# Performance work log

Measured on AMD Instinct MI355X. Metric: run time of the kernel, lower is better.

The kernel has to match this reference:

```python
import jax, jax.numpy as jnp
import numpy as np

B, T, H, L = 8, 256, 64, 3
NB, NF, HP = 17, 68, 6
K = 9  # temporal kernel
PAD = (K - 1) // 2
EPS = 1e-5


def _normalize(adj):
    adj = adj + np.eye(adj.shape[0], dtype=np.float32)
    d = adj.sum(1)
    dinv = np.power(d, -0.5)
    dinv[np.isinf(dinv)] = 0.0
    return (dinv[:, None] * adj * dinv[None, :]).astype(np.float32)


def _body_adj():
    a = np.zeros((NB, NB), np.float32)
    conns = [(0, 1), (0, 2), (1, 3), (2, 4), (0, 5), (0, 6), (5, 6), (5, 7), (7, 9), (6, 8), (8, 10), (5, 11), (6, 12), (11, 12), (11, 13), (13, 15), (12, 14), (14, 16)]
    for i, j in conns:
        a[i, j] = 1.0
        a[j, i] = 1.0
    return _normalize(a)


def _face_adj():
    a = np.zeros((NF, NF), np.float32)
    for i in range(16): a[i, i + 1] = 1.0
    for i in range(17, 21): a[i, i + 1] = 1.0
    for i in range(22, 26): a[i, i + 1] = 1.0
    for i in range(27, 30): a[i, i + 1] = 1.0
    for i in range(31, 35): a[i, i + 1] = 1.0
    for i in range(36, 41): a[i, i + 1] = 1.0
    a[41, 36] = 1.0
    for i in range(42, 47): a[i, i + 1] = 1.0
    a[47, 42] = 1.0
    for i in range(48, 59): a[i, i + 1] = 1.0
    a[59, 48] = 1.0
    for i in range(60, 67): a[i, i + 1] = 1.0
    a[67, 60] = 1.0
    a = a + a.T
    return _normalize(a)


def setup_inputs() -> dict:
    keys = iter(jax.random.split(jax.random.key(0), 80))

    def rn(shape, s):
        return jax.random.normal(next(keys), shape, jnp.float32) * s

    inp = {}
    inp['body_kps'] = jax.random.normal(next(keys), (B, T, NB * 2), jnp.float32)
    inp['face_kps_2d'] = jax.random.normal(next(keys), (B, T, NF * 2), jnp.float32)
    inp['head_pose'] = jax.random.normal(next(keys), (B, T, HP), jnp.float32)
    inp['body_adj'] = jnp.asarray(_body_adj())
    inp['face_adj'] = jnp.asarray(_face_adj())
    inp['body_proj_w'] = rn((2, H), 0.5)
    inp['body_proj_b'] = jnp.zeros((H,), jnp.float32)
    inp['face_proj_w'] = rn((2, H), 0.5)
    inp['face_proj_b'] = jnp.zeros((H,), jnp.float32)
    inp['head_w'] = rn((HP, H), 0.3)
    inp['head_b'] = jnp.zeros((H,), jnp.float32)
    for p in ('b', 'f'):
        inp[p + '_t1w'] = rn((L, H, H, K), 0.04)
        inp[p + '_t1b'] = jnp.zeros((L, H), jnp.float32)
        inp[p + '_bn1g'] = jnp.ones((L, H), jnp.float32)
        inp[p + '_bn1b'] = jnp.zeros((L, H), jnp.float32)
        inp[p + '_bn1m'] = rn((L, H), 0.1)
        inp[p + '_bn1v'] = jax.random.uniform(next(keys), (L, H), jnp.float32, 0.5, 1.5)
        inp[p + '_gcw'] = rn((L, H, H), 0.1)
        inp[p + '_gcb'] = jnp.zeros((L, H), jnp.float32)
        inp[p + '_t2w'] = rn((L, H, H, K), 0.04)
        inp[p + '_t2b'] = jnp.zeros((L, H), jnp.float32)
        inp[p + '_bn2g'] = jnp.ones((L, H), jnp.float32)
        inp[p + '_bn2b'] = jnp.zeros((L, H), jnp.float32)
        inp[p + '_bn2m'] = rn((L, H), 0.1)
        inp[p + '_bn2v'] = jax.random.uniform(next(keys), (L, H), jnp.float32, 0.5, 1.5)
    total = NB * H + NF * H + H  # 5504
    inp['fus1_w'] = rn((total, 4 * H), 0.02)
    inp['fus1_b'] = jnp.zeros((4 * H,), jnp.float32)
    inp['fus2_w'] = rn((4 * H, 2 * H), 0.06)
    inp['fus2_b'] = jnp.zeros((2 * H,), jnp.float32)
    inp['fus3_w'] = rn((2 * H, H), 0.09)
    inp['fus3_b'] = jnp.zeros((H,), jnp.float32)
    inp['fus4_w'] = rn((H, 5), 0.12)
    inp['fus4_b'] = jnp.zeros((5,), jnp.float32)
    return inp


def _conv_bn(x, w, b, g, be, m, v):
    # x: (BN, C, T); w: (O, I, K). Conv1d (pad=4) + eval-mode BatchNorm1d.
    y = jax.lax.conv_general_dilated(x, w, (1,), [(PAD, PAD)], dimension_numbers=('NCH', 'OIH', 'NCH'))
    y = y + b[None, :, None]
    inv = g * jax.lax.rsqrt(v + EPS)
    return y * inv[None, :, None] + (be - m * inv)[None, :, None]


def _block(x, adj, t1w, t1b, g1, b1, m1, v1, gw, gb, t2w, t2b, g2, b2, m2, v2):
    # x: (B, N, C, T); residual is identity (in_channels == out_channels)
    Bn, N, C, Tn = x.shape
    res = x
    h = jax.nn.relu(_conv_bn(x.reshape(Bn * N, C, Tn), t1w, t1b, g1, b1, m1, v1)).reshape(Bn, N, C, Tn)
    # spatial graph conv, batched over all timesteps at once (adj @ (x W) + b)
    support = jnp.einsum('bnct,co->bnot', h, gw)
    h = jax.nn.relu(jnp.einsum('mn,bnot->bmot', adj, support) + gb[None, None, :, None])
    h = _conv_bn(h.reshape(Bn * N, C, Tn), t2w, t2b, g2, b2, m2, v2).reshape(Bn, N, C, Tn)
    return h + res  # dropout = identity in eval


def _stream(x, n_nodes, pw, pb, adj, ps):
    Bn, Tn, _ = x.shape
    h = x.reshape(Bn, Tn, n_nodes, 2) @ pw + pb          # (B, T, N, H)
    h = jnp.transpose(h, (0, 2, 3, 1))                   # (B, N, H, T)
    for l in range(ps[0].shape[0]):
        h = _block(h, adj, *(p[l] for p in ps))
    return h.mean(axis=3).reshape(Bn, -1)                # temporal mean-pool, flatten nodes


def reference(body_kps, face_kps_2d, head_pose, body_adj, face_adj, body_proj_w, body_proj_b, face_proj_w, face_proj_b, head_w, head_b, b_t1w, b_t1b, b_bn1g, b_bn1b, b_bn1m, b_bn1v, b_gcw, b_gcb, b_t2w, b_t2b, b_bn2g, b_bn2b, b_bn2m, b_bn2v, f_t1w, f_t1b, f_bn1g, f_bn1b, f_bn1m, f_bn1v, f_gcw, f_gcb, f_t2w, f_t2b, f_bn2g, f_bn2b, f_bn2m, f_bn2v, fus1_w, fus1_b, fus2_w, fus2_b, fus3_w, fus3_b, fus4_w, fus4_b):
    bps = (b_t1w, b_t1b, b_bn1g, b_bn1b, b_bn1m, b_bn1v, b_gcw, b_gcb, b_t2w, b_t2b, b_bn2g, b_bn2b, b_bn2m, b_bn2v)
    fps = (f_t1w, f_t1b, f_bn1g, f_bn1b, f_bn1m, f_bn1v, f_gcw, f_gcb, f_t2w, f_t2b, f_bn2g, f_bn2b, f_bn2m, f_bn2v)
    bf = _stream(body_kps, NB, body_proj_w, body_proj_b, body_adj, bps)
    ff = _stream(face_kps_2d, NF, face_proj_w, face_proj_b, face_adj, fps)
    hp = jax.nn.relu(head_pose @ head_w + head_b).mean(axis=1)
    feat = jnp.concatenate([bf, ff, hp], axis=-1)
    h = jax.nn.relu(feat @ fus1_w + fus1_b)
    h = jax.nn.relu(h @ fus2_w + fus2_b)
    h = jax.nn.relu(h @ fus3_w + fus3_b)
    return h @ fus4_w + fus4_b
```

## Files before the change

kernel.cpp:

```cpp
#include <hip/hip_runtime.h>

constexpr int B_ = 8, T_ = 256, H_ = 64, L_ = 3, NB_ = 17, NF_ = 68, HP_ = 6, K_ = 9;
constexpr int FEAT_DIM = NB_ * H_ + NF_ * H_ + H_;
constexpr int HT = H_ * T_;

typedef _Float16 half4_t __attribute__((ext_vector_type(4)));
typedef _Float16 half8_t __attribute__((ext_vector_type(8)));
typedef float f32x16 __attribute__((ext_vector_type(16)));
typedef float f32x4 __attribute__((ext_vector_type(4)));

constexpr size_t SZ_AB = (size_t)B_ * NB_ * HT;
constexpr size_t SZ_AF = (size_t)B_ * NF_ * HT;
constexpr size_t OFF_TB   = 0;
constexpr size_t OFF_TF   = OFF_TB + SZ_AB / 2;
constexpr size_t OFF_SUPB = OFF_TF + SZ_AF / 2;
constexpr size_t OFF_SUPF = OFF_SUPB + SZ_AB / 2;
constexpr size_t OFF_GB   = OFF_SUPF + SZ_AF / 2;
constexpr size_t OFF_GF   = OFF_GB + SZ_AB / 2;
constexpr size_t OFF_W3   = OFF_GF + SZ_AF / 2;
constexpr size_t OFF_GW3  = OFF_W3 + 4 * 55296;
constexpr size_t OFF_B2   = OFF_GW3 + 2 * 6144;
constexpr size_t OFF_ADJPB= OFF_B2 + 768;
constexpr size_t OFF_ADJPF= OFF_ADJPB + 512;
constexpr size_t OFF_FEAT = OFF_ADJPF + 3840;
constexpr size_t OFF_P1   = OFF_FEAT + (size_t)B_ * FEAT_DIM;

struct ConvPrepSet { const float *w, *tb, *g, *bb, *m, *v; };

struct Args {
    const float *body_kps, *face_kps, *head_pose, *body_adj, *face_adj;
    const float *body_pw, *body_pb, *face_pw, *face_pb, *head_w, *head_b;
    ConvPrepSet sb1, sb2, sf1, sf2;
    const float *b_gcw, *f_gcw, *b_gcb, *f_gcb;
    const float *fus1_w, *fus1_b, *fus2_w, *fus2_b, *fus3_w, *fus3_b, *fus4_w, *fus4_b;
    _Float16 *TrB, *TrF, *SupB, *SupF, *Gb, *Gf;
    _Float16 *W3, *GW3, *adjPB, *adjPF;
    float *B2, *p1, *feat;
    float *out;
};

__device__ __forceinline__ half8_t ld_b8(const _Float16* p) {
    half4_t lo = *(const half4_t*)p;
    half4_t hi = *(const half4_t*)(p + 4);
    return __builtin_shufflevector(lo, hi, 0, 1, 2, 3, 4, 5, 6, 7);
}

__device__ __forceinline__ void st_b8(_Float16* p, half8_t v) {
    half4_t lo, hi;
#pragma unroll
    for (int j = 0; j < 4; ++j) { lo[j] = v[j]; hi[j] = v[4 + j]; }
    *(half4_t*)p = lo;
    *(half4_t*)(p + 4) = hi;
}

__device__ __forceinline__ void stage_chunk64(const _Float16* __restrict__ xb,
                                              _Float16* __restrict__ Xs, int tc, int tid) {
    for (int u = tid; u < 72 * 8; u += 256) {
        int row = u >> 3, c = u & 7;
        int t = tc * 64 + row - 4;
        half8_t v;
        if (t >= 0 && t < T_) {
            v = *(const half8_t*)(xb + (size_t)t * H_ + c * 8);
        } else {
#pragma unroll
            for (int j = 0; j < 8; ++j) v[j] = (_Float16)0.f;
        }
        st_b8(&Xs[row * 68 + c * 8], v);
    }
}

__device__ __forceinline__ void stage_res64(const _Float16* __restrict__ xb,
                                            _Float16* __restrict__ Rs, int tc, int tid) {
    for (int u = tid; u < 64 * 8; u += 256) {
        int row = u >> 3, c = u & 7;
        half8_t v = *(const half8_t*)(xb + (size_t)(tc * 64 + row) * H_ + c * 8);
        st_b8(&Rs[row * 68 + c * 8], v);
    }
}

__device__ __forceinline__ void conv_kloop(const half8_t* __restrict__ wl,
                                           const _Float16* __restrict__ Xs,
                                           int trow, int ln31, int kg, int ot,
                                           f32x16& acc) {
    const _Float16* xr0 = Xs + (size_t)(trow + ln31) * 68;
#pragma unroll
    for (int tap = 0; tap < K_; ++tap) {
#pragma unroll
        for (int ks = 0; ks < 4; ++ks) {
            int i8 = ks * 2 + kg;
            half8_t a = wl[(tap * 8 + i8) * H_ + ot * 32 + ln31];
            half8_t bf = ld_b8(xr0 + tap * 68 + i8 * 8);
            acc = __builtin_amdgcn_mfma_f32_32x32x16_f16(a, bf, acc, 0, 0, 0);
        }
    }
}

__device__ void convmix_core(const half8_t* __restrict__ wl,
                             const float* __restrict__ b1l,
                             const half8_t* __restrict__ gl,
                             _Float16* __restrict__ supb,
                             int tc, _Float16* __restrict__ Xs, int tid) {
    int ln = tid & 63;
    int w = __builtin_amdgcn_readfirstlane(tid >> 6);
    int ln31 = ln & 31, kg = ln >> 5;
    int ts = w & 1, ot = w >> 1;
    int trow = ts * 32;

    f32x16 acc;
#pragma unroll
    for (int r = 0; r < 16; ++r) acc[r] = 0.f;

    conv_kloop(wl, Xs, trow, ln31, kg, ot, acc);
    __syncthreads();

    _Float16* mrow = Xs + (size_t)(4 + trow + ln31) * 68;
#pragma unroll
    for (int rg = 0; rg < 4; ++rg) {
        int o0 = ot * 32 + rg * 8 + kg * 4;
        f32x4 bv = *(const f32x4*)(b1l + o0);
        half4_t hv;
#pragma unroll
        for (int j = 0; j < 4; ++j)
            hv[j] = (_Float16)fmaxf(acc[rg * 4 + j] + bv[j], 0.f);
        *(half4_t*)(mrow + o0) = hv;
    }
    __syncthreads();

    f32x16 acc2;
#pragma unroll
    for (int r = 0; r < 16; ++r) acc2[r] = 0.f;
#pragma unroll
    for (int ks = 0; ks < 4; ++ks) {
        int i8 = ks * 2 + kg;
        half8_t a = gl[i8 * H_ + ot * 32 + ln31];
        half8_t bf = ld_b8(mrow + i8 * 8);
        acc2 = __builtin_amdgcn_mfma_f32_32x32x16_f16(a, bf, acc2, 0, 0, 0);
    }
    __syncthreads();

#pragma unroll
    for (int rg = 0; rg < 4; ++rg) {
        int o0 = ot * 32 + rg * 8 + kg * 4;
        half4_t hv;
#pragma unroll
        for (int j = 0; j < 4; ++j)
            hv[j] = (_Float16)acc2[rg * 4 + j];
        *(half4_t*)(mrow + o0) = hv;
    }
    __syncthreads();
    _Float16* gout = supb + (size_t)(tc * 64) * H_;
    const _Float16* srow = Xs + 4 * 68;
#pragma unroll
    for (int k2 = 0; k2 < 2; ++k2) {
        int u = k2 * 256 + tid;
        int r = u >> 3, c = u & 7;
        half8_t v = ld_b8(srow + r * 68 + c * 8);
        *(half8_t*)(gout + (size_t)r * H_ + c * 8) = v;
    }
}

__global__ __launch_bounds__(256) void prep_k(Args A) {
    int blk = blockIdx.x;
    int tid = threadIdx.x;
    if (blk < 1728) {
        int set = blk / 432;
        int bx = blk % 432;
        ConvPrepSet s = (set == 0) ? A.sb1 : (set == 1) ? A.sb2 : (set == 2) ? A.sf1 : A.sf2;
        int idx = bx * 256 + tid;
        int k = idx % K_; int r = idx / K_;
        int i = r % H_; r /= H_;
        int o = r % H_; int l = r / H_;
        float sc = s.g[l * H_ + o] * rsqrtf(s.v[l * H_ + o] + 1e-5f);
        A.W3[(size_t)set * 110592 + ((((l * K_ + k) * 8 + (i >> 3)) * H_ + o) * 8) + (i & 7)]
            = (_Float16)(s.w[idx] * sc);
        if (i == 0 && k == 0)
            A.B2[set * 192 + l * H_ + o] =
                s.tb[l * H_ + o] * sc + s.bb[l * H_ + o] - s.m[l * H_ + o] * sc;
    } else if (blk < 1824) {
        int set = (blk - 1728) / 48;
        int bx = (blk - 1728) % 48;
        const float* gw = set ? A.f_gcw : A.b_gcw;
        int idx = bx * 256 + tid;
        int o = idx % H_; int r = idx / H_;
        int c = r % H_; int l = r / H_;
        A.GW3[(size_t)set * 12288 + (((l * 8 + (c >> 3)) * H_ + o) * 8) + (c & 7)]
            = (_Float16)gw[idx];
    } else {
        int idx = (blk - 1824) * 256 + tid;
        if (idx < 1024) {
            int m = idx >> 5, k = idx & 31;
            A.adjPB[idx] = (m < NB_ && k < NB_) ? (_Float16)A.body_adj[m * NB_ + k] : (_Float16)0.f;
        } else if (idx < 8704) {
            int j = idx - 1024;
            int m = j / 80, k = j % 80;
            A.adjPF[j] = (m < NF_ && k < NF_) ? (_Float16)A.face_adj[m * NF_ + k] : (_Float16)0.f;
        } else if (idx < 10752) {
            A.p1[idx - 8704] = 0.f;
        } else if (idx < 10752 + B_ * FEAT_DIM) {
            A.feat[idx - 10752] = 0.f;
        }
    }
}

__global__ __launch_bounds__(256, 8) void projcm_k(Args A) {
    __shared__ __align__(16) _Float16 Xs[72 * 68];
    int blk = blockIdx.x, tid = threadIdx.x;
    bool isB = blk < 4 * B_ * NB_;
    int j = isB ? blk : blk - 4 * B_ * NB_;
    int bn = j >> 2, tc = j & 3;
    const float* kps = isB ? A.body_kps : A.face_kps;
    const float* pw  = isB ? A.body_pw  : A.face_pw;
    const float* pb  = isB ? A.body_pb  : A.face_pb;
    _Float16* trunk  = isB ? A.TrB : A.TrF;
    int N = isB ? NB_ : NF_;
    int b = bn / N, n = bn % N;

    if (tid < 144) {
        int row = tid >> 1, hf = tid & 1;
        int t = tc * 64 + row - 4;
        _Float16* xr = Xs + row * 68 + hf * 32;
        if (t >= 0 && t < T_) {
            float x0 = kps[((size_t)b * T_ + t) * (N * 2) + n * 2 + 0];
            float x1 = kps[((size_t)b * T_ + t) * (N * 2) + n * 2 + 1];
            bool own = (row >= 4 && row < 68);
            _Float16* ob = trunk + (size_t)bn * HT + (size_t)t * H_ + hf * 32;
#pragma unroll
            for (int cg2 = 0; cg2 < 4; ++cg2) {
                half8_t v;
#pragma unroll
                for (int jj = 0; jj < 8; ++jj) {
                    int c = hf * 32 + cg2 * 8 + jj;
                    v[jj] = (_Float16)fmaf(x0, pw[c], fmaf(x1, pw[H_ + c], pb[c]));
                }
                st_b8(xr + cg2 * 8, v);
                if (own) *(half8_t*)(ob + cg2 * 8) = v;
            }
        } else {
            half8_t z;
#pragma unroll
            for (int jj = 0; jj < 8; ++jj) z[jj] = (_Float16)0.f;
            st_b8(xr, z);
            st_b8(xr + 8, z);
            st_b8(xr + 16, z);
            st_b8(xr + 24, z);
        }
    }
    __syncthreads();

    const half8_t* w1 = (const half8_t*)(A.W3 + (isB ? 0 : 221184));
    const float* b1l  = isB ? A.B2 : A.B2 + 384;
    const half8_t* gl = (const half8_t*)(A.GW3 + (isB ? 0 : 12288));
    _Float16* supb = (isB ? A.SupB : A.SupF) + (size_t)bn * HT;
    convmix_core(w1, b1l, gl, supb, tc, Xs, tid);
}

__global__ __launch_bounds__(256, 8) void cm_k(Args A, int l) {
    __shared__ __align__(16) _Float16 Xs[72 * 68];
    int blk = blockIdx.x, tid = threadIdx.x;
    bool isB = blk < 4 * B_ * NB_;
    int j = isB ? blk : blk - 4 * B_ * NB_;
    int bn = j >> 2, tc = j & 3;
    const _Float16* trunk = isB ? A.TrB : A.TrF;

    stage_chunk64(trunk + (size_t)bn * HT, Xs, tc, tid);
    __syncthreads();

    const half8_t* w1 = (const half8_t*)(A.W3 + (isB ? 0 : 221184)) + (size_t)l * (K_ * 8 * H_);
    const float* b1l  = (isB ? A.B2 : A.B2 + 384) + l * H_;
    const half8_t* gl = (const half8_t*)(A.GW3 + (isB ? 0 : 12288)) + (size_t)l * (8 * H_);
    _Float16* supb = (isB ? A.SupB : A.SupF) + (size_t)bn * HT;
    convmix_core(w1, b1l, gl, supb, tc, Xs, tid);
}

template <int N, int MT, int KS>
__device__ void adjmix_impl(const _Float16* __restrict__ sup,
                            const half8_t* __restrict__ adjP,
                            const float* __restrict__ gb,
                            _Float16* __restrict__ out,
                            int blk, int l, _Float16* Ls, int tid) {
    constexpr int KP = KS * 16;
    constexpr int PITCH = KP + 4;
    int b = blk >> 7, cb = blk & 127;
    int colbase = cb * 128;

    for (int u = tid; u < KP * 16; u += 256) {
        int n = u >> 4, cs = u & 15;
        half8_t v;
        if (n < N) v = *(const half8_t*)(sup + (size_t)(b * N + n) * HT + colbase + cs * 8);
        else {
#pragma unroll
            for (int j = 0; j < 8; ++j) v[j] = (_Float16)0.f;
        }
#pragma unroll
        for (int j = 0; j < 8; ++j) Ls[(cs * 8 + j) * PITCH + n] = v[j];
    }
    __syncthreads();

    int ln = tid & 63;
    int w = __builtin_amdgcn_readfirstlane(tid >> 6);
    int ln31 = ln & 31, kg = ln >> 5;
    int colL = w * 32 + ln31;

    f32x16 acc[MT];
#pragma unroll
    for (int mt = 0; mt < MT; ++mt)
#pragma unroll
        for (int r = 0; r < 16; ++r) acc[mt][r] = 0.f;

#pragma unroll
    for (int ks = 0; ks < KS; ++ks) {
        half8_t bf = ld_b8(&Ls[colL * PITCH + ks * 16 + kg * 8]);
#pragma unroll
        for (int mt = 0; mt < MT; ++mt) {
            half8_t af = adjP[(size_t)(mt * 32 + ln31) * (KP / 8) + ks * 2 + kg];
            acc[mt] = __builtin_amdgcn_mfma_f32_32x32x16_f16(af, bf, acc[mt], 0, 0, 0);
        }
    }
    __syncthreads();

    float gbv = gb[l * H_ + (colL & 63)];
#pragma unroll
    for (int mt = 0; mt < MT; ++mt) {
#pragma unroll
        for (int r = 0; r < 16; ++r) {
            int m = mt * 32 + (r & 3) + 8 * (r >> 2) + 4 * kg;
            Ls[m * 132 + colL] = (_Float16)fmaxf(acc[mt][r] + gbv, 0.f);
        }
    }
    __syncthreads();

    for (int u = tid; u < N * 16; u += 256) {
        int m = u >> 4, c = u & 15;
        half8_t v = ld_b8(&Ls[m * 132 + c * 8]);
        *(half8_t*)(out + (size_t)(b * N + m) * HT + colbase + c * 8) = v;
    }
}

__global__ __launch_bounds__(256) void adjmix_k(Args A, int l) {
    __shared__ __align__(16) _Float16 Ls[12800];
    int blk = blockIdx.x, tid = threadIdx.x;
    if (blk < 1024)
        adjmix_impl<NB_, 1, 2>(A.SupB, (const half8_t*)A.adjPB, A.b_gcb, A.Gb, blk, l, Ls, tid);
    else
        adjmix_impl<NF_, 3, 5>(A.SupF, (const half8_t*)A.adjPF, A.f_gcb, A.Gf, blk - 1024, l, Ls, tid);
}

__global__ __launch_bounds__(256, 8) void c2_k(Args A, int l) {
    __shared__ __align__(16) _Float16 Xs[72 * 68];
    __shared__ __align__(16) _Float16 Rs[64 * 68];
    int blk = blockIdx.x, tid = threadIdx.x;
    bool isB = blk < 4 * B_ * NB_;
    int j = isB ? blk : blk - 4 * B_ * NB_;
    int bn = j >> 2, tc = j & 3;
    const _Float16* G = isB ? A.Gb : A.Gf;
    _Float16* trunk   = isB ? A.TrB : A.TrF;
    const half8_t* w2 = (const half8_t*)(A.W3 + (isB ? 110592 : 331776)) + (size_t)l * (K_ * 8 * H_);
    const float* b2l  = (isB ? A.B2 + 192 : A.B2 + 576) + l * H_;

    stage_chunk64(G + (size_t)bn * HT, Xs, tc, tid);
    stage_res64(trunk + (size_t)bn * HT, Rs, tc, tid);
    __syncthreads();

    int ln = tid & 63;
    int w = __builtin_amdgcn_readfirstlane(tid >> 6);
    int ln31 = ln & 31, kg = ln >> 5;
    int ts = w & 1, ot = w >> 1;
    int trow = ts * 32;

    f32x16 acc;
#pragma unroll
    for (int r = 0; r < 16; ++r) acc[r] = 0.f;

    conv_kloop(w2, Xs, trow, ln31, kg, ot, acc);
    __syncthreads();

    {
        _Float16* orow = Xs + (size_t)(4 + trow + ln31) * 68;
        const _Float16* rrow = Rs + (size_t)(trow + ln31) * 68;
#pragma unroll
        for (int rg = 0; rg < 4; ++rg) {
            int o0 = ot * 32 + rg * 8 + kg * 4;
            f32x4 bv = *(const f32x4*)(b2l + o0);
            half4_t rv = *(const half4_t*)(rrow + o0);
            half4_t hv;
#pragma unroll
            for (int jj = 0; jj < 4; ++jj)
                hv[jj] = (_Float16)(acc[rg * 4 + jj] + bv[jj] + (float)rv[jj]);
            *(half4_t*)(orow + o0) = hv;
        }
    }
    __syncthreads();

    _Float16* gout = trunk + (size_t)bn * HT + (size_t)(tc * 64) * H_;
    const _Float16* srow = Xs + 4 * 68;
#pragma unroll
    for (int k2 = 0; k2 < 2; ++k2) {
        int u = k2 * 256 + tid;
        int r = u >> 3, c = u & 7;
        half8_t v = ld_b8(srow + r * 68 + c * 8);
        *(half8_t*)(gout + (size_t)r * H_ + c * 8) = v;
    }
}

__global__ __launch_bounds__(256, 8) void c2last_k(Args A) {
    __shared__ __align__(16) _Float16 Xs[72 * 68];
    __shared__ __align__(16) _Float16 Rs[64 * 68];
    int blk = blockIdx.x, tid = threadIdx.x;
    if (blk >= 2720) {
        int b = blk - 2720;
        if (tid < 64) {
            int c = tid;
            float w0 = A.head_w[c], w1 = A.head_w[64 + c], w2 = A.head_w[128 + c],
                  w3 = A.head_w[192 + c], w4 = A.head_w[256 + c], w5 = A.head_w[320 + c];
            float bias = A.head_b[c];
            float acc = 0.f;
            for (int t = 0; t < T_; ++t) {
                const float* xr = A.head_pose + ((size_t)b * T_ + t) * HP_;
                float s = fmaf(xr[0], w0, fmaf(xr[1], w1, fmaf(xr[2], w2,
                          fmaf(xr[3], w3, fmaf(xr[4], w4, fmaf(xr[5], w5, bias))))));
                acc += fmaxf(s, 0.f);
            }
            A.feat[(size_t)b * FEAT_DIM + NB_ * H_ + NF_ * H_ + c] = acc * (1.f / 256.f);
        }
        return;
    }
    constexpr int l = L_ - 1;
    bool isB = blk < 4 * B_ * NB_;
    int j = isB ? blk : blk - 4 * B_ * NB_;
    int bn = j >> 2, tc = j & 3;
    const _Float16* G = isB ? A.Gb : A.Gf;
    _Float16* trunk   = isB ? A.TrB : A.TrF;
    const half8_t* w2 = (const half8_t*)(A.W3 + (isB ? 110592 : 331776)) + (size_t)l * (K_ * 8 * H_);
    const float* b2l  = (isB ? A.B2 + 192 : A.B2 + 576) + l * H_;
    int N = isB ? NB_ : NF_;
    int fbase = isB ? 0 : NB_ * H_;

    stage_chunk64(G + (size_t)bn * HT, Xs, tc, tid);
    stage_res64(trunk + (size_t)bn * HT, Rs, tc, tid);
    __syncthreads();

    int ln = tid & 63;
    int w = __builtin_amdgcn_readfirstlane(tid >> 6);
    int ln31 = ln & 31, kg = ln >> 5;
    int ts = w & 1, ot = w >> 1;
    int trow = ts * 32;

    f32x16 acc;
#pragma unroll
    for (int r = 0; r < 16; ++r) acc[r] = 0.f;

    conv_kloop(w2, Xs, trow, ln31, kg, ot, acc);

    float sv[16];
    const _Float16* rrow = Rs + (size_t)(trow + ln31) * 68;
#pragma unroll
    for (int rg = 0; rg < 4; ++rg) {
        int o0 = ot * 32 + rg * 8 + kg * 4;
        f32x4 bv = *(const f32x4*)(b2l + o0);
        half4_t rv = *(const half4_t*)(rrow + o0);
#pragma unroll
        for (int jj = 0; jj < 4; ++jj) {
            int r = rg * 4 + jj;
            float s = acc[r] + bv[jj] + (float)rv[jj];
#pragma unroll
            for (int off = 1; off < 32; off <<= 1) s += __shfl_xor(s, off);
            sv[r] = s;
        }
    }
    __syncthreads();
    float* red = (float*)Xs;
    if (ln31 == 0) {
#pragma unroll
        for (int r = 0; r < 16; ++r) {
            int olocal = (r & 3) + 8 * (r >> 2) + 4 * kg;
            red[w * 32 + olocal] = sv[r];
        }
    }
    __syncthreads();
    if (tid < 64) {
        int o = tid, ot2 = o >> 5, ol = o & 31;
        float s = red[(ot2 * 2) * 32 + ol] + red[(ot2 * 2 + 1) * 32 + ol];
        int b = bn / N, n = bn % N;
        atomicAdd(&A.feat[(size_t)b * FEAT_DIM + fbase + n * H_ + o], s * (1.f / 256.f));
    }
}

__global__ __launch_bounds__(256) void fus1_k(Args A) {
    __shared__ float fv[8][64];
    int blk = blockIdx.x;
    int ic = blk >> 1, kh = blk & 1;
    int base = ic * 128 + kh * 64;
    int tid = threadIdx.x;
    for (int u = tid; u < 8 * 64; u += 256) {
        int b = u >> 6, j = u & 63;
        fv[b][j] = A.feat[(size_t)b * FEAT_DIM + base + j];
    }
    __syncthreads();
    float acc[8];
#pragma unroll
    for (int b = 0; b < 8; ++b) acc[b] = 0.f;
    const float* wb = A.fus1_w + (size_t)base * 256 + tid;
    for (int i = 0; i < 64; ++i) {
        float wv = wb[(size_t)i * 256];
#pragma unroll
        for (int b = 0; b < 8; ++b) acc[b] = fmaf(fv[b][i], wv, acc[b]);
    }
#pragma unroll
    for (int b = 0; b < 8; ++b) atomicAdd(&A.p1[b * 256 + tid], acc[b]);
}

__global__ __launch_bounds__(256) void fus_tail_k(Args A) {
    __shared__ float s1[256], s2[128], s3[64];
    int b = blockIdx.x, tid = threadIdx.x;
    s1[tid] = fmaxf(A.p1[b * 256 + tid] + A.fus1_b[tid], 0.f);
    __syncthreads();
    if (tid < 128) {
        float acc = A.fus2_b[tid];
        for (int i = 0; i < 256; ++i) acc = fmaf(s1[i], A.fus2_w[i * 128 + tid], acc);
        s2[tid] = fmaxf(acc, 0.f);
    }
    __syncthreads();
    if (tid < 64) {
        float acc = A.fus3_b[tid];
        for (int i = 0; i < 128; ++i) acc = fmaf(s2[i], A.fus3_w[i * 64 + tid], acc);
        s3[tid] = fmaxf(acc, 0.f);
    }
    __syncthreads();
    if (tid < 5) {
        float acc = A.fus4_b[tid];
        for (int i = 0; i < 64; ++i) acc = fmaf(s3[i], A.fus4_w[i * 5 + tid], acc);
        A.out[b * 5 + tid] = acc;
    }
}

extern "C" void kernel_launch(void* const* d_in, const int* in_sizes, int n_in,
                              void* d_out, int out_size, void* d_ws, size_t ws_size,
                              hipStream_t stream) {
    float* ws = (float*)d_ws;

    Args A;
    A.body_kps = (const float*)d_in[0];
    A.face_kps = (const float*)d_in[1];
    A.head_pose = (const float*)d_in[2];
    A.body_adj = (const float*)d_in[3];
    A.face_adj = (const float*)d_in[4];
    A.body_pw = (const float*)d_in[5];
    A.body_pb = (const float*)d_in[6];
    A.face_pw = (const float*)d_in[7];
    A.face_pb = (const float*)d_in[8];
    A.head_w = (const float*)d_in[9];
    A.head_b = (const float*)d_in[10];
    A.sb1 = ConvPrepSet{(const float*)d_in[11], (const float*)d_in[12], (const float*)d_in[13],
                        (const float*)d_in[14], (const float*)d_in[15], (const float*)d_in[16]};
    A.b_gcw = (const float*)d_in[17];
    A.b_gcb = (const float*)d_in[18];
    A.sb2 = ConvPrepSet{(const float*)d_in[19], (const float*)d_in[20], (const float*)d_in[21],
                        (const float*)d_in[22], (const float*)d_in[23], (const float*)d_in[24]};
    A.sf1 = ConvPrepSet{(const float*)d_in[25], (const float*)d_in[26], (const float*)d_in[27],
                        (const float*)d_in[28], (const float*)d_in[29], (const float*)d_in[30]};
    A.f_gcw = (const float*)d_in[31];
    A.f_gcb = (const float*)d_in[32];
    A.sf2 = ConvPrepSet{(const float*)d_in[33], (const float*)d_in[34], (const float*)d_in[35],
                        (const float*)d_in[36], (const float*)d_in[37], (const float*)d_in[38]};
    A.fus1_w = (const float*)d_in[39]; A.fus1_b = (const float*)d_in[40];
    A.fus2_w = (const float*)d_in[41]; A.fus2_b = (const float*)d_in[42];
    A.fus3_w = (const float*)d_in[43]; A.fus3_b = (const float*)d_in[44];
    A.fus4_w = (const float*)d_in[45]; A.fus4_b = (const float*)d_in[46];

    A.TrB  = (_Float16*)(ws + OFF_TB);
    A.TrF  = (_Float16*)(ws + OFF_TF);
    A.SupB = (_Float16*)(ws + OFF_SUPB);
    A.SupF = (_Float16*)(ws + OFF_SUPF);
    A.Gb   = (_Float16*)(ws + OFF_GB);
    A.Gf   = (_Float16*)(ws + OFF_GF);
    A.W3   = (_Float16*)(ws + OFF_W3);
    A.GW3  = (_Float16*)(ws + OFF_GW3);
    A.adjPB= (_Float16*)(ws + OFF_ADJPB);
    A.adjPF= (_Float16*)(ws + OFF_ADJPF);
    A.B2   = ws + OFF_B2;
    A.feat = ws + OFF_FEAT;
    A.p1   = ws + OFF_P1;
    A.out  = (float*)d_out;

    const int gconv = 4 * (B_ * NB_ + B_ * NF_);

    prep_k<<<2038, 256, 0, stream>>>(A);
    projcm_k<<<gconv, 256, 0, stream>>>(A);
    for (int l = 0; l < L_; ++l) {
        adjmix_k<<<2048, 256, 0, stream>>>(A, l);
        if (l < L_ - 1) {
            c2_k<<<gconv, 256, 0, stream>>>(A, l);
            cm_k<<<gconv, 256, 0, stream>>>(A, l + 1);
        } else {
            c2last_k<<<gconv + 8, 256, 0, stream>>>(A);
        }
    }
    fus1_k<<<86, 256, 0, stream>>>(A);
    fus_tail_k<<<8, 256, 0, stream>>>(A);
}
```

Measured before the change: 372.8 us.

## Loop all four time chunks per block with register-prefetched staging

```diff
diff --git a/kernel.cpp b/kernel.cpp
--- a/kernel.cpp
+++ b/kernel.cpp
@@ -53,29 +53,45 @@
     *(half4_t*)(p + 4) = hi;
 }
 
-__device__ __forceinline__ void stage_chunk64(const _Float16* __restrict__ xb,
-                                              _Float16* __restrict__ Xs, int tc, int tid) {
-    for (int u = tid; u < 72 * 8; u += 256) {
-        int row = u >> 3, c = u & 7;
-        int t = tc * 64 + row - 4;
-        half8_t v;
-        if (t >= 0 && t < T_) {
-            v = *(const half8_t*)(xb + (size_t)t * H_ + c * 8);
-        } else {
-#pragma unroll
-            for (int j = 0; j < 8; ++j) v[j] = (_Float16)0.f;
-        }
-        st_b8(&Xs[row * 68 + c * 8], v);
-    }
-}
-
-__device__ __forceinline__ void stage_res64(const _Float16* __restrict__ xb,
-                                            _Float16* __restrict__ Rs, int tc, int tid) {
-    for (int u = tid; u < 64 * 8; u += 256) {
-        int row = u >> 3, c = u & 7;
-        half8_t v = *(const half8_t*)(xb + (size_t)(tc * 64 + row) * H_ + c * 8);
-        st_b8(&Rs[row * 68 + c * 8], v);
-    }
+struct SReg { half8_t v[3]; };
+
+__device__ __forceinline__ void issue_stage(const _Float16* __restrict__ xb, int tc, int tid,
+                                            SReg& S) {
+#pragma unroll
+    for (int k = 0; k < 3; ++k) {
+        int u = k * 256 + tid;
+        if (u < 576) {
+            int row = u >> 3, c = u & 7;
+            int t = tc * 64 + row - 4;
+            if (t >= 0 && t < T_) {
+                S.v[k] = *(const half8_t*)(xb + (size_t)t * H_ + c * 8);
+            } else {
+#pragma unroll
+                for (int j = 0; j < 8; ++j) S.v[k][j] = (_Float16)0.f;
+            }
+        }
+    }
+}
+
+__device__ __forceinline__ void write_stage(_Float16* __restrict__ Xs, int tid, const SReg& S) {
+#pragma unroll
+    for (int k = 0; k < 3; ++k) {
+        int u = k * 256 + tid;
+        if (u < 576) {
+            int row = u >> 3, c = u & 7;
+            st_b8(&Xs[row * 68 + c * 8], S.v[k]);
+        }
+    }
+}
+
+struct RReg { half4_t r[4]; };
+
+__device__ __forceinline__ void issue_res(const _Float16* __restrict__ tb, int tc, int trow,
+                                          int ln31, int kg, int ot, RReg& R) {
+    const _Float16* rr = tb + (size_t)(tc * 64 + trow + ln31) * H_ + ot * 32 + kg * 4;
+#pragma unroll
+    for (int rg = 0; rg < 4; ++rg)
+        R.r[rg] = *(const half4_t*)(rr + rg * 8);
 }
 
 __device__ __forceinline__ void conv_kloop(const half8_t* __restrict__ wl,
@@ -202,74 +218,89 @@
     }
 }
 
-__global__ __launch_bounds__(256, 8) void projcm_k(Args A) {
+__global__ __launch_bounds__(256, 4) void projcm_k(Args A) {
     __shared__ __align__(16) _Float16 Xs[72 * 68];
     int blk = blockIdx.x, tid = threadIdx.x;
-    bool isB = blk < 4 * B_ * NB_;
-    int j = isB ? blk : blk - 4 * B_ * NB_;
-    int bn = j >> 2, tc = j & 3;
+    bool isB = blk < B_ * NB_;
+    int bn = isB ? blk : blk - B_ * NB_;
     const float* kps = isB ? A.body_kps : A.face_kps;
     const float* pw  = isB ? A.body_pw  : A.face_pw;
     const float* pb  = isB ? A.body_pb  : A.face_pb;
-    _Float16* trunk  = isB ? A.TrB : A.TrF;
+    _Float16* trunk  = (isB ? A.TrB : A.TrF) + (size_t)bn * HT;
     int N = isB ? NB_ : NF_;
     int b = bn / N, n = bn % N;
-
-    if (tid < 144) {
-        int row = tid >> 1, hf = tid & 1;
-        int t = tc * 64 + row - 4;
-        _Float16* xr = Xs + row * 68 + hf * 32;
-        if (t >= 0 && t < T_) {
-            float x0 = kps[((size_t)b * T_ + t) * (N * 2) + n * 2 + 0];
-            float x1 = kps[((size_t)b * T_ + t) * (N * 2) + n * 2 + 1];
-            bool own = (row >= 4 && row < 68);
-            _Float16* ob = trunk + (size_t)bn * HT + (size_t)t * H_ + hf * 32;
-#pragma unroll
-            for (int cg2 = 0; cg2 < 4; ++cg2) {
-                half8_t v;
-#pragma unroll
-                for (int jj = 0; jj < 8; ++jj) {
-                    int c = hf * 32 + cg2 * 8 + jj;
-                    v[jj] = (_Float16)fmaf(x0, pw[c], fmaf(x1, pw[H_ + c], pb[c]));
-                }
-                st_b8(xr + cg2 * 8, v);
-                if (own) *(half8_t*)(ob + cg2 * 8) = v;
-            }
-        } else {
-            half8_t z;
-#pragma unroll
-            for (int jj = 0; jj < 8; ++jj) z[jj] = (_Float16)0.f;
-            st_b8(xr, z);
-            st_b8(xr + 8, z);
-            st_b8(xr + 16, z);
-            st_b8(xr + 24, z);
-        }
-    }
-    __syncthreads();
 
     const half8_t* w1 = (const half8_t*)(A.W3 + (isB ? 0 : 221184));
     const float* b1l  = isB ? A.B2 : A.B2 + 384;
     const half8_t* gl = (const half8_t*)(A.GW3 + (isB ? 0 : 12288));
     _Float16* supb = (isB ? A.SupB : A.SupF) + (size_t)bn * HT;
-    convmix_core(w1, b1l, gl, supb, tc, Xs, tid);
-}
-
-__global__ __launch_bounds__(256, 8) void cm_k(Args A, int l) {
+
+#pragma unroll
+    for (int tc = 0; tc < 4; ++tc) {
+        if (tid < 144) {
+            int row = tid >> 1, hf = tid & 1;
+            int t = tc * 64 + row - 4;
+            _Float16* xr = Xs + row * 68 + hf * 32;
+            if (t >= 0 && t < T_) {
+                float x0 = kps[((size_t)b * T_ + t) * (N * 2) + n * 2 + 0];
+                float x1 = kps[((size_t)b * T_ + t) * (N * 2) + n * 2 + 1];
+                bool own = (row >= 4 && row < 68);
+                _Float16* ob = trunk + (size_t)t * H_ + hf * 32;
+#pragma unroll
+                for (int cg2 = 0; cg2 < 4; ++cg2) {
+                    half8_t v;
+#pragma unroll
+                    for (int jj = 0; jj < 8; ++jj) {
+                        int c = hf * 32 + cg2 * 8 + jj;
+                        v[jj] = (_Float16)fmaf(x0, pw[c], fmaf(x1, pw[H_ + c], pb[c]));
+                    }
+                    st_b8(xr + cg2 * 8, v);
+                    if (own) *(half8_t*)(ob + cg2 * 8) = v;
+                }
+            } else {
+                half8_t z;
+#pragma unroll
+                for (int jj = 0; jj < 8; ++jj) z[jj] = (_Float16)0.f;
+                st_b8(xr, z);
+                st_b8(xr + 8, z);
+                st_b8(xr + 16, z);
+                st_b8(xr + 24, z);
+            }
+        }
+        __syncthreads();
+        convmix_core(w1, b1l, gl, supb, tc, Xs, tid);
+        __syncthreads();
+    }
+}
+
+__global__ __launch_bounds__(256, 4) void cm_k(Args A, int l) {
     __shared__ __align__(16) _Float16 Xs[72 * 68];
     int blk = blockIdx.x, tid = threadIdx.x;
-    bool isB = blk < 4 * B_ * NB_;
-    int j = isB ? blk : blk - 4 * B_ * NB_;
-    int bn = j >> 2, tc = j & 3;
-    const _Float16* trunk = isB ? A.TrB : A.TrF;
-
-    stage_chunk64(trunk + (size_t)bn * HT, Xs, tc, tid);
-    __syncthreads();
+    bool isB = blk < B_ * NB_;
+    int bn = isB ? blk : blk - B_ * NB_;
+    const _Float16* trunk = (isB ? A.TrB : A.TrF) + (size_t)bn * HT;
 
     const half8_t* w1 = (const half8_t*)(A.W3 + (isB ? 0 : 221184)) + (size_t)l * (K_ * 8 * H_);
     const float* b1l  = (isB ? A.B2 : A.B2 + 384) + l * H_;
     const half8_t* gl = (const half8_t*)(A.GW3 + (isB ? 0 : 12288)) + (size_t)l * (8 * H_);
     _Float16* supb = (isB ? A.SupB : A.SupF) + (size_t)bn * HT;
-    convmix_core(w1, b1l, gl, supb, tc, Xs, tid);
+
+    SReg S;
+    issue_stage(trunk, 0, tid, S);
+    write_stage(Xs, tid, S);
+    __syncthreads();
+
+#pragma unroll
+    for (int tc = 0; tc < 4; ++tc) {
+        SReg Sn;
+        if (tc < 3) issue_stage(trunk, tc + 1, tid, Sn);
+        convmix_core(w1, b1l, gl, supb, tc, Xs, tid);
+        __syncthreads();
+        if (tc < 3) {
+            write_stage(Xs, tid, Sn);
+            __syncthreads();
+        }
+    }
 }
 
 template <int N, int MT, int KS>
@@ -277,10 +308,9 @@
                             const half8_t* __restrict__ adjP,
                             const float* __restrict__ gb,
                             _Float16* __restrict__ out,
-                            int blk, int l, _Float16* Ls, int tid) {
+                            int b, int cb, int l, _Float16* Ls, int tid) {
     constexpr int KP = KS * 16;
     constexpr int PITCH = KP + 4;
-    int b = blk >> 7, cb = blk & 127;
     int colbase = cb * 128;
 
     for (int u = tid; u < KP * 16; u += 256) {
@@ -339,27 +369,23 @@
 __global__ __launch_bounds__(256) void adjmix_k(Args A, int l) {
     __shared__ __align__(16) _Float16 Ls[12800];
     int blk = blockIdx.x, tid = threadIdx.x;
-    if (blk < 1024)
-        adjmix_impl<NB_, 1, 2>(A.SupB, (const half8_t*)A.adjPB, A.b_gcb, A.Gb, blk, l, Ls, tid);
+    int b = blk & 7;
+    int u = blk >> 3;
+    if (u < 128)
+        adjmix_impl<NB_, 1, 2>(A.SupB, (const half8_t*)A.adjPB, A.b_gcb, A.Gb, b, u, l, Ls, tid);
     else
-        adjmix_impl<NF_, 3, 5>(A.SupF, (const half8_t*)A.adjPF, A.f_gcb, A.Gf, blk - 1024, l, Ls, tid);
-}
-
-__global__ __launch_bounds__(256, 8) void c2_k(Args A, int l) {
+        adjmix_impl<NF_, 3, 5>(A.SupF, (const half8_t*)A.adjPF, A.f_gcb, A.Gf, b, u - 128, l, Ls, tid);
+}
+
+__global__ __launch_bounds__(256, 4) void c2_k(Args A, int l) {
     __shared__ __align__(16) _Float16 Xs[72 * 68];
-    __shared__ __align__(16) _Float16 Rs[64 * 68];
     int blk = blockIdx.x, tid = threadIdx.x;
-    bool isB = blk < 4 * B_ * NB_;
-    int j = isB ? blk : blk - 4 * B_ * NB_;
-    int bn = j >> 2, tc = j & 3;
-    const _Float16* G = isB ? A.Gb : A.Gf;
-    _Float16* trunk   = isB ? A.TrB : A.TrF;
+    bool isB = blk < B_ * NB_;
+    int bn = isB ? blk : blk - B_ * NB_;
+    const _Float16* G = (isB ? A.Gb : A.Gf) + (size_t)bn * HT;
+    _Float16* trunk   = (isB ? A.TrB : A.TrF) + (size_t)bn * HT;
     const half8_t* w2 = (const half8_t*)(A.W3 + (isB ? 110592 : 331776)) + (size_t)l * (K_ * 8 * H_);
     const float* b2l  = (isB ? A.B2 + 192 : A.B2 + 576) + l * H_;
-
-    stage_chunk64(G + (size_t)bn * HT, Xs, tc, tid);
-    stage_res64(trunk + (size_t)bn * HT, Rs, tc, tid);
-    __syncthreads();
 
     int ln = tid & 63;
     int w = __builtin_amdgcn_readfirstlane(tid >> 6);
@@ -367,47 +393,62 @@
     int ts = w & 1, ot = w >> 1;
     int trow = ts * 32;
 
-    f32x16 acc;
-#pragma unroll
-    for (int r = 0; r < 16; ++r) acc[r] = 0.f;
-
-    conv_kloop(w2, Xs, trow, ln31, kg, ot, acc);
-    __syncthreads();
-
-    {
-        _Float16* orow = Xs + (size_t)(4 + trow + ln31) * 68;
-        const _Float16* rrow = Rs + (size_t)(trow + ln31) * 68;
-#pragma unroll
-        for (int rg = 0; rg < 4; ++rg) {
-            int o0 = ot * 32 + rg * 8 + kg * 4;
-            f32x4 bv = *(const f32x4*)(b2l + o0);
-            half4_t rv = *(const half4_t*)(rrow + o0);
-            half4_t hv;
-#pragma unroll
-            for (int jj = 0; jj < 4; ++jj)
-                hv[jj] = (_Float16)(acc[rg * 4 + jj] + bv[jj] + (float)rv[jj]);
-            *(half4_t*)(orow + o0) = hv;
-        }
-    }
-    __syncthreads();
-
-    _Float16* gout = trunk + (size_t)bn * HT + (size_t)(tc * 64) * H_;
-    const _Float16* srow = Xs + 4 * 68;
-#pragma unroll
-    for (int k2 = 0; k2 < 2; ++k2) {
-        int u = k2 * 256 + tid;
-        int r = u >> 3, c = u & 7;
-        half8_t v = ld_b8(srow + r * 68 + c * 8);
-        *(half8_t*)(gout + (size_t)r * H_ + c * 8) = v;
-    }
-}
-
-__global__ __launch_bounds__(256, 8) void c2last_k(Args A) {
+    SReg S;
+    issue_stage(G, 0, tid, S);
+    write_stage(Xs, tid, S);
+    __syncthreads();
+
+#pragma unroll
+    for (int tc = 0; tc < 4; ++tc) {
+        RReg R;
+        issue_res(trunk, tc, trow, ln31, kg, ot, R);
+        SReg Sn;
+        if (tc < 3) issue_stage(G, tc + 1, tid, Sn);
+
+        f32x16 acc;
+#pragma unroll
+        for (int r = 0; r < 16; ++r) acc[r] = 0.f;
+        conv_kloop(w2, Xs, trow, ln31, kg, ot, acc);
+        __syncthreads();
+
+        {
+            _Float16* orow = Xs + (size_t)(4 + trow + ln31) * 68;
+#pragma unroll
+            for (int rg = 0; rg < 4; ++rg) {
+                int o0 = ot * 32 + rg * 8 + kg * 4;
+                f32x4 bv = *(const f32x4*)(b2l + o0);
+                half4_t rv = R.r[rg];
+                half4_t hv;
+#pragma unroll
+                for (int jj = 0; jj < 4; ++jj)
+                    hv[jj] = (_Float16)(acc[rg * 4 + jj] + bv[jj] + (float)rv[jj]);
+                *(half4_t*)(orow + o0) = hv;
+            }
+        }
+        __syncthreads();
+
+        _Float16* gout = trunk + (size_t)(tc * 64) * H_;
+        const _Float16* srow = Xs + 4 * 68;
+#pragma unroll
+        for (int k2 = 0; k2 < 2; ++k2) {
+            int u = k2 * 256 + tid;
+            int r = u >> 3, c = u & 7;
+            half8_t v = ld_b8(srow + r * 68 + c * 8);
+            *(half8_t*)(gout + (size_t)r * H_ + c * 8) = v;
+        }
+        __syncthreads();
+        if (tc < 3) {
+            write_stage(Xs, tid, Sn);
+            __syncthreads();
+        }
+    }
+}
+
+__global__ __launch_bounds__(256, 4) void c2last_k(Args A) {
     __shared__ __align__(16) _Float16 Xs[72 * 68];
-    __shared__ __align__(16) _Float16 Rs[64 * 68];
     int blk = blockIdx.x, tid = threadIdx.x;
-    if (blk >= 2720) {
-        int b = blk - 2720;
+    if (blk >= 680) {
+        int b = blk - 680;
         if (tid < 64) {
             int c = tid;
             float w0 = A.head_w[c], w1 = A.head_w[64 + c], w2 = A.head_w[128 + c],
@@ -425,19 +466,15 @@
         return;
     }
     constexpr int l = L_ - 1;
-    bool isB = blk < 4 * B_ * NB_;
-    int j = isB ? blk : blk - 4 * B_ * NB_;
-    int bn = j >> 2, tc = j & 3;
-    const _Float16* G = isB ? A.Gb : A.Gf;
-    _Float16* trunk   = isB ? A.TrB : A.TrF;
+    bool isB = blk < B_ * NB_;
+    int bn = isB ? blk : blk - B_ * NB_;
+    const _Float16* G = (isB ? A.Gb : A.Gf) + (size_t)bn * HT;
+    const _Float16* trunk = (isB ? A.TrB : A.TrF) + (size_t)bn * HT;
     const half8_t* w2 = (const half8_t*)(A.W3 + (isB ? 110592 : 331776)) + (size_t)l * (K_ * 8 * H_);
     const float* b2l  = (isB ? A.B2 + 192 : A.B2 + 576) + l * H_;
     int N = isB ? NB_ : NF_;
     int fbase = isB ? 0 : NB_ * H_;
-
-    stage_chunk64(G + (size_t)bn * HT, Xs, tc, tid);
-    stage_res64(trunk + (size_t)bn * HT, Rs, tc, tid);
-    __syncthreads();
+    int b = bn / N, n = bn % N;
 
     int ln = tid & 63;
     int w = __builtin_amdgcn_readfirstlane(tid >> 6);
@@ -445,42 +482,60 @@
     int ts = w & 1, ot = w >> 1;
     int trow = ts * 32;
 
-    f32x16 acc;
-#pragma unroll
-    for (int r = 0; r < 16; ++r) acc[r] = 0.f;
-
-    conv_kloop(w2, Xs, trow, ln31, kg, ot, acc);
-
-    float sv[16];
-    const _Float16* rrow = Rs + (size_t)(trow + ln31) * 68;
-#pragma unroll
-    for (int rg = 0; rg < 4; ++rg) {
-        int o0 = ot * 32 + rg * 8 + kg * 4;
-        f32x4 bv = *(const f32x4*)(b2l + o0);
-        half4_t rv = *(const half4_t*)(rrow + o0);
-#pragma unroll
-        for (int jj = 0; jj < 4; ++jj) {
-            int r = rg * 4 + jj;
-            float s = acc[r] + bv[jj] + (float)rv[jj];
-#pragma unroll
-            for (int off = 1; off < 32; off <<= 1) s += __shfl_xor(s, off);
-            sv[r] = s;
-        }
-    }
-    __syncthreads();
+    SReg S;
+    issue_stage(G, 0, tid, S);
+    write_stage(Xs, tid, S);
+    __syncthreads();
+
+    float svacc[16];
+#pragma unroll
+    for (int r = 0; r < 16; ++r) svacc[r] = 0.f;
+
+#pragma unroll
+    for (int tc = 0; tc < 4; ++tc) {
+        RReg R;
+        issue_res(trunk, tc, trow, ln31, kg, ot, R);
+        SReg Sn;
+        if (tc < 3) issue_stage(G, tc + 1, tid, Sn);
+
+        f32x16 acc;
+#pragma unroll
+        for (int r = 0; r < 16; ++r) acc[r] = 0.f;
+        conv_kloop(w2, Xs, trow, ln31, kg, ot, acc);
+
+#pragma unroll
+        for (int rg = 0; rg < 4; ++rg) {
+            int o0 = ot * 32 + rg * 8 + kg * 4;
+            f32x4 bv = *(const f32x4*)(b2l + o0);
+            half4_t rv = R.r[rg];
+#pragma unroll
+            for (int jj = 0; jj < 4; ++jj) {
+                int r = rg * 4 + jj;
+                float s = acc[r] + bv[jj] + (float)rv[jj];
+#pragma unroll
+                for (int off = 1; off < 32; off <<= 1) s += __shfl_xor(s, off);
+                svacc[r] += s;
+            }
+        }
+        __syncthreads();
+        if (tc < 3) {
+            write_stage(Xs, tid, Sn);
+            __syncthreads();
+        }
+    }
+
     float* red = (float*)Xs;
     if (ln31 == 0) {
 #pragma unroll
         for (int r = 0; r < 16; ++r) {
             int olocal = (r & 3) + 8 * (r >> 2) + 4 * kg;
-            red[w * 32 + olocal] = sv[r];
+            red[w * 32 + olocal] = svacc[r];
         }
     }
     __syncthreads();
     if (tid < 64) {
         int o = tid, ot2 = o >> 5, ol = o & 31;
         float s = red[(ot2 * 2) * 32 + ol] + red[(ot2 * 2 + 1) * 32 + ol];
-        int b = bn / N, n = bn % N;
         atomicAdd(&A.feat[(size_t)b * FEAT_DIM + fbase + n * H_ + o], s * (1.f / 256.f));
     }
 }
@@ -582,7 +637,7 @@
     A.p1   = ws + OFF_P1;
     A.out  = (float*)d_out;
 
-    const int gconv = 4 * (B_ * NB_ + B_ * NF_);
+    const int gconv = B_ * NB_ + B_ * NF_;
 
     prep_k<<<2038, 256, 0, stream>>>(A);
     projcm_k<<<gconv, 256, 0, stream>>>(A);
```

After: 476.1 us. 27.7% more time.
